# Optimization experiments

Hardware: AMD Instinct MI355X
Metric: run time of the kernel (lower is better)

Reference implementation:

```python
import jax, jax.numpy as jnp
import numpy as np
from jax import lax

CH = 256          # channels
FACTOR = 32       # EMA groups
CG = CH // FACTOR # channels per group = 8
B = 8             # number of point-cloud segments (batch)
NPTS = 32768      # points per segment (equal-length segments)
N = B * NPTS
EPS = 1e-5        # GroupNorm eps
FUSION_W = 0.1


def setup_inputs() -> dict:
    key = jax.random.key(0)
    ks = jax.random.split(key, 6)
    feat = jax.random.normal(ks[0], (N, CH), dtype=jnp.float32)
    # cumulative offsets of equal-length segments
    offset = ((jnp.arange(B, dtype=jnp.int32) + 1) * NPTS)
    s1 = 1.0 / np.sqrt(CG)      # torch Conv1d default init scale (fan_in=CG*k)
    s3 = 1.0 / np.sqrt(CG * 3)
    conv1_w = jax.random.uniform(ks[1], (CG, CG, 1), jnp.float32, -s1, s1)
    conv1_b = jax.random.uniform(ks[2], (CG,), jnp.float32, -s1, s1)
    conv3_w = jax.random.uniform(ks[3], (CG, CG, 3), jnp.float32, -s3, s3)
    conv3_b = jax.random.uniform(ks[4], (CG,), jnp.float32, -s3, s3)
    gn_w = jnp.ones((CG,), jnp.float32)
    gn_b = jnp.zeros((CG,), jnp.float32)
    fusion_weight = jnp.float32(FUSION_W)
    return {"feat": feat, "conv1_w": conv1_w, "conv1_b": conv1_b,
            "conv3_w": conv3_w, "conv3_b": conv3_b,
            "gn_w": gn_w, "gn_b": gn_b,
            "fusion_weight": fusion_weight, "offset": offset}


def _ema(x, conv1_w, conv1_b, conv3_w, conv3_b, gn_w, gn_b):
    # x: [BG, CG, n]  (BG = B * FACTOR)
    x_g = x.mean(-1, keepdims=True)                                   # agp -> [BG, CG, 1]
    x_g = jnp.einsum('oi,bis->bos', conv1_w[:, :, 0], x_g) + conv1_b[None, :, None]
    h = x * jax.nn.sigmoid(x_g)
    # GroupNorm(CG, CG): per-channel normalization over the point axis
    mu = h.mean(-1, keepdims=True)
    var = h.var(-1, keepdims=True)
    x1 = (h - mu) * lax.rsqrt(var + EPS) * gn_w[None, :, None] + gn_b[None, :, None]
    # conv3x3 along points, padding 1
    x2 = lax.conv_general_dilated(x, conv3_w, (1,), [(1, 1)],
                                  dimension_numbers=('NCH', 'OIH', 'NCH'))
    x2 = x2 + conv3_b[None, :, None]
    x11 = jax.nn.softmax(x1.mean(-1), axis=-1)                        # [BG, CG]
    x21 = jax.nn.softmax(x2.mean(-1), axis=-1)                        # [BG, CG]
    w = jnp.einsum('bc,bcn->bn', x11, x2) + jnp.einsum('bc,bcn->bn', x21, x1)
    return x * jax.nn.sigmoid(w)[:, None, :]


def reference(feat, conv1_w, conv1_b, conv3_w, conv3_b, gn_w, gn_b, fusion_weight, offset):
    # equal-length segments: [N, CH] -> [B, CH, NPTS]
    x = feat.reshape(B, NPTS, CH).transpose(0, 2, 1)
    gx = x.reshape(B * FACTOR, CG, NPTS)
    x_ema = _ema(gx, conv1_w, conv1_b, conv3_w, conv3_b, gn_w, gn_b).reshape(B, CH, NPTS)
    out = x + fusion_weight * (x_ema - x)      # residual fusion
    return out.transpose(0, 2, 1).reshape(N, CH)
```

## Files before the change

### kernel.cpp

```cpp
#include <hip/hip_runtime.h>
#include <math.h>

#define NSEG 8
#define NPTS 32768
#define CH   256
#define CG   8
#define EPS_GN 1e-5f


__global__ __launch_bounds__(256) void k_zero(float* __restrict__ acc) {
  acc[blockIdx.x * 256 + threadIdx.x] = 0.0f;
}

__global__ __launch_bounds__(256) void k_reduce(const float* __restrict__ feat,
                                                float* __restrict__ accS,
                                                float* __restrict__ accS2) {
  const int blk   = blockIdx.x;
  const int seg   = blk >> 7;
  const int chunk = blk & 127;
  const int q  = threadIdx.x & 63;
  const int dr = threadIdx.x >> 6;
  const float4* f4 = (const float4*)feat;
  const size_t rowbase = (size_t)seg * NPTS + (size_t)chunk * 256;
  float4 s  = make_float4(0.f, 0.f, 0.f, 0.f);
  float4 s2 = make_float4(0.f, 0.f, 0.f, 0.f);
  for (int r = dr; r < 256; r += 4) {
    float4 v = f4[(rowbase + r) * (CH / 4) + q];
    s.x += v.x;     s.y += v.y;     s.z += v.z;     s.w += v.w;
    s2.x += v.x*v.x; s2.y += v.y*v.y; s2.z += v.z*v.z; s2.w += v.w*v.w;
  }
  __shared__ float4 rs[256];
  __shared__ float4 rq[256];
  rs[threadIdx.x] = s;
  rq[threadIdx.x] = s2;
  __syncthreads();
  if (threadIdx.x < 64) {
    float4 a = rs[q], b = rs[64 + q], c = rs[128 + q], d = rs[192 + q];
    float4 e = rq[q], f = rq[64 + q], g = rq[128 + q], h = rq[192 + q];
    float sx = a.x + b.x + c.x + d.x;
    float sy = a.y + b.y + c.y + d.y;
    float sz = a.z + b.z + c.z + d.z;
    float sw = a.w + b.w + c.w + d.w;
    float tx = e.x + f.x + g.x + h.x;
    float ty = e.y + f.y + g.y + h.y;
    float tz = e.z + f.z + g.z + h.z;
    float tw = e.w + f.w + g.w + h.w;
    float* pS  = accS  + seg * CH + q * 4;
    float* pS2 = accS2 + seg * CH + q * 4;
    atomicAdd(pS + 0, sx);  atomicAdd(pS + 1, sy);
    atomicAdd(pS + 2, sz);  atomicAdd(pS + 3, sw);
    atomicAdd(pS2 + 0, tx); atomicAdd(pS2 + 1, ty);
    atomicAdd(pS2 + 2, tz); atomicAdd(pS2 + 3, tw);
  }
}

__global__ __launch_bounds__(256) void k_coef(const float* __restrict__ feat,
                                              const float* __restrict__ accS,
                                              const float* __restrict__ accS2,
                                              const float* __restrict__ c1w,
                                              const float* __restrict__ c1b,
                                              const float* __restrict__ c3w,
                                              const float* __restrict__ c3b,
                                              const float* __restrict__ gnw,
                                              const float* __restrict__ gnb,
                                              float* __restrict__ coeff) {
  const int gb  = threadIdx.x;
  const int seg = gb >> 5;
  const int g   = gb & 31;
  const float invn = 1.0f / (float)NPTS;

  float S[8], S2[8], mean[8], var[8];
#pragma unroll
  for (int i = 0; i < 8; ++i) {
    S[i]  = accS [seg * CH + g * 8 + i];
    S2[i] = accS2[seg * CH + g * 8 + i];
    mean[i] = S[i] * invn;
    var[i]  = fmaxf(S2[i] * invn - mean[i] * mean[i], 0.0f);
  }
  float xf[8], xl[8];
  const size_t rowf = ((size_t)seg * NPTS) * CH + g * 8;
  const size_t rowl = ((size_t)seg * NPTS + (NPTS - 1)) * CH + g * 8;
#pragma unroll
  for (int i = 0; i < 8; ++i) { xf[i] = feat[rowf + i]; xl[i] = feat[rowl + i]; }

  float a1[8];
#pragma unroll
  for (int o = 0; o < 8; ++o) {
    float xg = c1b[o];
#pragma unroll
    for (int i = 0; i < 8; ++i) xg += c1w[o * 8 + i] * mean[i];
    float gate = 1.0f / (1.0f + expf(-xg));
    float inv  = rsqrtf(gate * gate * var[o] + EPS_GN);
    a1[o] = gate * inv * gnw[o];
  }

  float x2m[8];
#pragma unroll
  for (int o = 0; o < 8; ++o) {
    float t = 0.0f;
#pragma unroll
    for (int i = 0; i < 8; ++i) {
      const float w0 = c3w[o * 24 + i * 3 + 0];
      const float w1 = c3w[o * 24 + i * 3 + 1];
      const float w2 = c3w[o * 24 + i * 3 + 2];
      t += w0 * (S[i] - xl[i]) + w1 * S[i] + w2 * (S[i] - xf[i]);
    }
    x2m[o] = c3b[o] + t * invn;
  }

  float x11[8], x21[8];
  {
    float m1 = gnb[0], m2 = x2m[0];
#pragma unroll
    for (int o = 1; o < 8; ++o) { m1 = fmaxf(m1, gnb[o]); m2 = fmaxf(m2, x2m[o]); }
    float d1 = 0.0f, d2 = 0.0f;
#pragma unroll
    for (int o = 0; o < 8; ++o) {
      x11[o] = expf(gnb[o] - m1); d1 += x11[o];
      x21[o] = expf(x2m[o] - m2); d2 += x21[o];
    }
    d1 = 1.0f / d1; d2 = 1.0f / d2;
#pragma unroll
    for (int o = 0; o < 8; ++o) { x11[o] *= d1; x21[o] *= d2; }
  }

  float P[8], Q[8], R[8];
#pragma unroll
  for (int i = 0; i < 8; ++i) {
    float p = 0.0f, qc = 0.0f, rr = 0.0f;
#pragma unroll
    for (int o = 0; o < 8; ++o) {
      const float s11 = x11[o];
      p  += s11 * c3w[o * 24 + i * 3 + 0];
      qc += s11 * c3w[o * 24 + i * 3 + 1];
      rr += s11 * c3w[o * 24 + i * 3 + 2];
    }
    P[i] = p; Q[i] = qc + x21[i] * a1[i]; R[i] = rr;
  }
  float K = 0.0f;
#pragma unroll
  for (int o = 0; o < 8; ++o)
    K += x11[o] * c3b[o] + x21[o] * (gnb[o] - a1[o] * mean[o]);

  float* cp = coeff + gb * 32;
  cp[0] = K;
#pragma unroll
  for (int i = 0; i < 8; ++i) { cp[4 + i] = P[i]; cp[12 + i] = Q[i]; cp[20 + i] = R[i]; }
}

__global__ __launch_bounds__(256) void k_main(const float* __restrict__ feat,
                                              const float* __restrict__ coeff,
                                              const float* __restrict__ fwp,
                                              float* __restrict__ out) {
  const int blk   = blockIdx.x;
  const int seg   = blk >> 8;
  const int chunk = blk & 255;
  const int g  = threadIdx.x & 31;
  const int dr = threadIdx.x >> 5;
  const int gb = seg * 32 + g;

  const float4* cp = (const float4*)(coeff + gb * 32);
  const float4 c0 = cp[0];
  const float4 P0 = cp[1], P1 = cp[2];
  const float4 Q0 = cp[3], Q1 = cp[4];
  const float4 R0 = cp[5], R1 = cp[6];
  const float K  = c0.x;
  const float fw = fwp[0];
  const float w1 = 1.0f - fw;

  const int r0 = chunk * 128;
  for (int r = r0 + dr; r < r0 + 128; r += 8) {
    const size_t row = (size_t)seg * NPTS + r;
    const float4* xp0 = (const float4*)(feat + row * CH + g * 8);
    const float4 a0 = xp0[0], a1 = xp0[1];
    float w = K
      + Q0.x * a0.x + Q0.y * a0.y + Q0.z * a0.z + Q0.w * a0.w
      + Q1.x * a1.x + Q1.y * a1.y + Q1.z * a1.z + Q1.w * a1.w;
    if (r > 0) {
      const float4* xm = xp0 - (CH / 4);
      const float4 m0 = xm[0], m1 = xm[1];
      w += P0.x * m0.x + P0.y * m0.y + P0.z * m0.z + P0.w * m0.w
         + P1.x * m1.x + P1.y * m1.y + P1.z * m1.z + P1.w * m1.w;
    }
    if (r < NPTS - 1) {
      const float4* xq = xp0 + (CH / 4);
      const float4 p0 = xq[0], p1 = xq[1];
      w += R0.x * p0.x + R0.y * p0.y + R0.z * p0.z + R0.w * p0.w
         + R1.x * p1.x + R1.y * p1.y + R1.z * p1.z + R1.w * p1.w;
    }
    const float sig   = 1.0f / (1.0f + __expf(-w));
    const float scale = w1 + fw * sig;
    float4 o0 = make_float4(a0.x * scale, a0.y * scale, a0.z * scale, a0.w * scale);
    float4 o1 = make_float4(a1.x * scale, a1.y * scale, a1.z * scale, a1.w * scale);
    float4* op = (float4*)(out + row * CH + g * 8);
    op[0] = o0; op[1] = o1;
  }
}

extern "C" void kernel_launch(void* const* d_in, const int* in_sizes, int n_in,
                              void* d_out, int out_size, void* d_ws, size_t ws_size,
                              hipStream_t stream) {
  const float* feat = (const float*)d_in[0];
  const float* c1w  = (const float*)d_in[1];
  const float* c1b  = (const float*)d_in[2];
  const float* c3w  = (const float*)d_in[3];
  const float* c3b  = (const float*)d_in[4];
  const float* gnw  = (const float*)d_in[5];
  const float* gnb  = (const float*)d_in[6];
  const float* fwp  = (const float*)d_in[7];
  float* out = (float*)d_out;
  float* ws  = (float*)d_ws;
  float* accS  = ws;
  float* accS2 = ws + NSEG * CH;
  float* coeff = ws + 2 * NSEG * CH;

  k_zero  <<<16,   256, 0, stream>>>(ws);
  k_reduce<<<1024, 256, 0, stream>>>(feat, accS, accS2);
  k_coef  <<<1,    256, 0, stream>>>(feat, accS, accS2, c1w, c1b, c3w, c3b, gnw, gnb, coeff);
  k_main  <<<2048, 256, 0, stream>>>(feat, coeff, fwp, out);
}
```

Before: 567.4 us.

## Replace atomic reduction with partial sums and stream rows with neighbor reuse

The reduction kernel now writes per-block partial sums to workspace instead of issuing atomics, which removes the zeroing kernel. A parallel coefficient kernel with one block per segment then sums those partials. The main kernel gives each thread a run of 16 consecutive rows and carries the previous and next row's dot products in registers, so each row is loaded about once rather than three times. The cost is a 4 MB partial buffer, a serial 256-step loop in the coefficient kernel, and access patterns where each warp touches different rows.

```diff
diff --git a/kernel.cpp b/kernel.cpp
--- a/kernel.cpp
+++ b/kernel.cpp
@@ -4,30 +4,27 @@
 #define NSEG 8
 #define NPTS 32768
 #define CH   256
-#define CG   8
 #define EPS_GN 1e-5f
 
 
-__global__ __launch_bounds__(256) void k_zero(float* __restrict__ acc) {
-  acc[blockIdx.x * 256 + threadIdx.x] = 0.0f;
+__device__ __forceinline__ float dot8(float4 a0, float4 a1, float4 b0, float4 b1) {
+  return a0.x * b0.x + a0.y * b0.y + a0.z * b0.z + a0.w * b0.w
+       + a1.x * b1.x + a1.y * b1.y + a1.z * b1.z + a1.w * b1.w;
 }
 
 __global__ __launch_bounds__(256) void k_reduce(const float* __restrict__ feat,
-                                                float* __restrict__ accS,
-                                                float* __restrict__ accS2) {
-  const int blk   = blockIdx.x;
-  const int seg   = blk >> 7;
-  const int chunk = blk & 127;
+                                                float* __restrict__ part) {
+  const int blk = blockIdx.x;
   const int q  = threadIdx.x & 63;
   const int dr = threadIdx.x >> 6;
   const float4* f4 = (const float4*)feat;
-  const size_t rowbase = (size_t)seg * NPTS + (size_t)chunk * 256;
+  const size_t rowbase = (size_t)blk * 128;
   float4 s  = make_float4(0.f, 0.f, 0.f, 0.f);
   float4 s2 = make_float4(0.f, 0.f, 0.f, 0.f);
-  for (int r = dr; r < 256; r += 4) {
+  for (int r = dr; r < 128; r += 4) {
     float4 v = f4[(rowbase + r) * (CH / 4) + q];
-    s.x += v.x;     s.y += v.y;     s.z += v.z;     s.w += v.w;
-    s2.x += v.x*v.x; s2.y += v.y*v.y; s2.z += v.z*v.z; s2.w += v.w*v.w;
+    s.x  += v.x;       s.y  += v.y;       s.z  += v.z;       s.w  += v.w;
+    s2.x += v.x * v.x; s2.y += v.y * v.y; s2.z += v.z * v.z; s2.w += v.w * v.w;
   }
   __shared__ float4 rs[256];
   __shared__ float4 rq[256];
@@ -37,26 +34,18 @@
   if (threadIdx.x < 64) {
     float4 a = rs[q], b = rs[64 + q], c = rs[128 + q], d = rs[192 + q];
     float4 e = rq[q], f = rq[64 + q], g = rq[128 + q], h = rq[192 + q];
-    float sx = a.x + b.x + c.x + d.x;
-    float sy = a.y + b.y + c.y + d.y;
-    float sz = a.z + b.z + c.z + d.z;
-    float sw = a.w + b.w + c.w + d.w;
-    float tx = e.x + f.x + g.x + h.x;
-    float ty = e.y + f.y + g.y + h.y;
-    float tz = e.z + f.z + g.z + h.z;
-    float tw = e.w + f.w + g.w + h.w;
-    float* pS  = accS  + seg * CH + q * 4;
-    float* pS2 = accS2 + seg * CH + q * 4;
-    atomicAdd(pS + 0, sx);  atomicAdd(pS + 1, sy);
-    atomicAdd(pS + 2, sz);  atomicAdd(pS + 3, sw);
-    atomicAdd(pS2 + 0, tx); atomicAdd(pS2 + 1, ty);
-    atomicAdd(pS2 + 2, tz); atomicAdd(pS2 + 3, tw);
+    float4 S  = make_float4(a.x + b.x + c.x + d.x, a.y + b.y + c.y + d.y,
+                            a.z + b.z + c.z + d.z, a.w + b.w + c.w + d.w);
+    float4 S2 = make_float4(e.x + f.x + g.x + h.x, e.y + f.y + g.y + h.y,
+                            e.z + f.z + g.z + h.z, e.w + f.w + g.w + h.w);
+    float4* pp = (float4*)(part + (size_t)blk * 512);
+    pp[q]      = S;
+    pp[64 + q] = S2;
   }
 }
 
 __global__ __launch_bounds__(256) void k_coef(const float* __restrict__ feat,
-                                              const float* __restrict__ accS,
-                                              const float* __restrict__ accS2,
+                                              const float* __restrict__ part,
                                               const float* __restrict__ c1w,
                                               const float* __restrict__ c1b,
                                               const float* __restrict__ c3w,
@@ -64,88 +53,94 @@
                                               const float* __restrict__ gnw,
                                               const float* __restrict__ gnb,
                                               float* __restrict__ coeff) {
-  const int gb  = threadIdx.x;
-  const int seg = gb >> 5;
-  const int g   = gb & 31;
-  const float invn = 1.0f / (float)NPTS;
-
-  float S[8], S2[8], mean[8], var[8];
-#pragma unroll
-  for (int i = 0; i < 8; ++i) {
-    S[i]  = accS [seg * CH + g * 8 + i];
-    S2[i] = accS2[seg * CH + g * 8 + i];
-    mean[i] = S[i] * invn;
-    var[i]  = fmaxf(S2[i] * invn - mean[i] * mean[i], 0.0f);
-  }
-  float xf[8], xl[8];
-  const size_t rowf = ((size_t)seg * NPTS) * CH + g * 8;
-  const size_t rowl = ((size_t)seg * NPTS + (NPTS - 1)) * CH + g * 8;
-#pragma unroll
-  for (int i = 0; i < 8; ++i) { xf[i] = feat[rowf + i]; xl[i] = feat[rowl + i]; }
-
-  float a1[8];
-#pragma unroll
-  for (int o = 0; o < 8; ++o) {
-    float xg = c1b[o];
-#pragma unroll
-    for (int i = 0; i < 8; ++i) xg += c1w[o * 8 + i] * mean[i];
-    float gate = 1.0f / (1.0f + expf(-xg));
-    float inv  = rsqrtf(gate * gate * var[o] + EPS_GN);
-    a1[o] = gate * inv * gnw[o];
-  }
-
-  float x2m[8];
-#pragma unroll
-  for (int o = 0; o < 8; ++o) {
-    float t = 0.0f;
+  const int seg = blockIdx.x;
+  const int c   = threadIdx.x;
+  const float* pb = part + (size_t)seg * 256 * 512;
+  float S = 0.0f, S2 = 0.0f;
+  for (int p = 0; p < 256; ++p) {
+    S  += pb[(size_t)p * 512 + c];
+    S2 += pb[(size_t)p * 512 + 256 + c];
+  }
+  __shared__ float sS[256], sS2[256], sxf[256], sxl[256];
+  sS[c]  = S;
+  sS2[c] = S2;
+  sxf[c] = feat[(size_t)seg * NPTS * CH + c];
+  sxl[c] = feat[((size_t)seg * NPTS + (NPTS - 1)) * CH + c];
+  __syncthreads();
+
+  if (c < 32) {
+    const int g = c;
+    const float invn = 1.0f / (float)NPTS;
+    float Ss[8], Q2[8], mean[8], var[8], xf[8], xl[8];
 #pragma unroll
     for (int i = 0; i < 8; ++i) {
-      const float w0 = c3w[o * 24 + i * 3 + 0];
-      const float w1 = c3w[o * 24 + i * 3 + 1];
-      const float w2 = c3w[o * 24 + i * 3 + 2];
-      t += w0 * (S[i] - xl[i]) + w1 * S[i] + w2 * (S[i] - xf[i]);
-    }
-    x2m[o] = c3b[o] + t * invn;
-  }
-
-  float x11[8], x21[8];
-  {
-    float m1 = gnb[0], m2 = x2m[0];
-#pragma unroll
-    for (int o = 1; o < 8; ++o) { m1 = fmaxf(m1, gnb[o]); m2 = fmaxf(m2, x2m[o]); }
-    float d1 = 0.0f, d2 = 0.0f;
+      Ss[i] = sS [g * 8 + i];
+      Q2[i] = sS2[g * 8 + i];
+      mean[i] = Ss[i] * invn;
+      var[i]  = fmaxf(Q2[i] * invn - mean[i] * mean[i], 0.0f);
+      xf[i] = sxf[g * 8 + i];
+      xl[i] = sxl[g * 8 + i];
+    }
+    float a1[8];
 #pragma unroll
     for (int o = 0; o < 8; ++o) {
-      x11[o] = expf(gnb[o] - m1); d1 += x11[o];
-      x21[o] = expf(x2m[o] - m2); d2 += x21[o];
-    }
-    d1 = 1.0f / d1; d2 = 1.0f / d2;
-#pragma unroll
-    for (int o = 0; o < 8; ++o) { x11[o] *= d1; x21[o] *= d2; }
-  }
-
-  float P[8], Q[8], R[8];
-#pragma unroll
-  for (int i = 0; i < 8; ++i) {
-    float p = 0.0f, qc = 0.0f, rr = 0.0f;
+      float xg = c1b[o];
+#pragma unroll
+      for (int i = 0; i < 8; ++i) xg += c1w[o * 8 + i] * mean[i];
+      float gate = 1.0f / (1.0f + expf(-xg));
+      a1[o] = gate * rsqrtf(gate * gate * var[o] + EPS_GN) * gnw[o];
+    }
+    float x2m[8];
 #pragma unroll
     for (int o = 0; o < 8; ++o) {
-      const float s11 = x11[o];
-      p  += s11 * c3w[o * 24 + i * 3 + 0];
-      qc += s11 * c3w[o * 24 + i * 3 + 1];
-      rr += s11 * c3w[o * 24 + i * 3 + 2];
-    }
-    P[i] = p; Q[i] = qc + x21[i] * a1[i]; R[i] = rr;
-  }
-  float K = 0.0f;
-#pragma unroll
-  for (int o = 0; o < 8; ++o)
-    K += x11[o] * c3b[o] + x21[o] * (gnb[o] - a1[o] * mean[o]);
-
-  float* cp = coeff + gb * 32;
-  cp[0] = K;
-#pragma unroll
-  for (int i = 0; i < 8; ++i) { cp[4 + i] = P[i]; cp[12 + i] = Q[i]; cp[20 + i] = R[i]; }
+      float t = 0.0f;
+#pragma unroll
+      for (int i = 0; i < 8; ++i) {
+        const float w0 = c3w[o * 24 + i * 3 + 0];
+        const float w1 = c3w[o * 24 + i * 3 + 1];
+        const float w2 = c3w[o * 24 + i * 3 + 2];
+        t += w0 * (Ss[i] - xl[i]) + w1 * Ss[i] + w2 * (Ss[i] - xf[i]);
+      }
+      x2m[o] = c3b[o] + t * invn;
+    }
+    float x11[8], x21[8];
+    {
+      float m1 = gnb[0], m2 = x2m[0];
+#pragma unroll
+      for (int o = 1; o < 8; ++o) { m1 = fmaxf(m1, gnb[o]); m2 = fmaxf(m2, x2m[o]); }
+      float d1 = 0.0f, d2 = 0.0f;
+#pragma unroll
+      for (int o = 0; o < 8; ++o) {
+        x11[o] = expf(gnb[o] - m1); d1 += x11[o];
+        x21[o] = expf(x2m[o] - m2); d2 += x21[o];
+      }
+      d1 = 1.0f / d1; d2 = 1.0f / d2;
+#pragma unroll
+      for (int o = 0; o < 8; ++o) { x11[o] *= d1; x21[o] *= d2; }
+    }
+    float P[8], Qc[8], R[8];
+#pragma unroll
+    for (int i = 0; i < 8; ++i) {
+      float p = 0.0f, qq = 0.0f, rr = 0.0f;
+#pragma unroll
+      for (int o = 0; o < 8; ++o) {
+        const float s11 = x11[o];
+        p  += s11 * c3w[o * 24 + i * 3 + 0];
+        qq += s11 * c3w[o * 24 + i * 3 + 1];
+        rr += s11 * c3w[o * 24 + i * 3 + 2];
+      }
+      P[i] = p; Qc[i] = qq + x21[i] * a1[i]; R[i] = rr;
+    }
+    float K = 0.0f;
+#pragma unroll
+    for (int o = 0; o < 8; ++o)
+      K += x11[o] * c3b[o] + x21[o] * (gnb[o] - a1[o] * mean[o]);
+
+    float* cpw = coeff + (seg * 32 + g) * 32;
+    cpw[0] = K;
+#pragma unroll
+    for (int i = 0; i < 8; ++i) { cpw[4 + i] = P[i]; cpw[12 + i] = Qc[i]; cpw[20 + i] = R[i]; }
+  }
 }
 
 __global__ __launch_bounds__(256) void k_main(const float* __restrict__ feat,
@@ -156,7 +151,7 @@
   const int seg   = blk >> 8;
   const int chunk = blk & 255;
   const int g  = threadIdx.x & 31;
-  const int dr = threadIdx.x >> 5;
+  const int tr = threadIdx.x >> 5;
   const int gb = seg * 32 + g;
 
   const float4* cp = (const float4*)(coeff + gb * 32);
@@ -168,32 +163,36 @@
   const float fw = fwp[0];
   const float w1 = 1.0f - fw;
 
-  const int r0 = chunk * 128;
-  for (int r = r0 + dr; r < r0 + 128; r += 8) {
-    const size_t row = (size_t)seg * NPTS + r;
-    const float4* xp0 = (const float4*)(feat + row * CH + g * 8);
-    const float4 a0 = xp0[0], a1 = xp0[1];
-    float w = K
-      + Q0.x * a0.x + Q0.y * a0.y + Q0.z * a0.z + Q0.w * a0.w
-      + Q1.x * a1.x + Q1.y * a1.y + Q1.z * a1.z + Q1.w * a1.w;
-    if (r > 0) {
-      const float4* xm = xp0 - (CH / 4);
-      const float4 m0 = xm[0], m1 = xm[1];
-      w += P0.x * m0.x + P0.y * m0.y + P0.z * m0.z + P0.w * m0.w
-         + P1.x * m1.x + P1.y * m1.y + P1.z * m1.z + P1.w * m1.w;
-    }
-    if (r < NPTS - 1) {
-      const float4* xq = xp0 + (CH / 4);
-      const float4 p0 = xq[0], p1 = xq[1];
-      w += R0.x * p0.x + R0.y * p0.y + R0.z * p0.z + R0.w * p0.w
-         + R1.x * p1.x + R1.y * p1.y + R1.z * p1.z + R1.w * p1.w;
-    }
-    const float sig   = 1.0f / (1.0f + __expf(-w));
-    const float scale = w1 + fw * sig;
-    float4 o0 = make_float4(a0.x * scale, a0.y * scale, a0.z * scale, a0.w * scale);
-    float4 o1 = make_float4(a1.x * scale, a1.y * scale, a1.z * scale, a1.w * scale);
-    float4* op = (float4*)(out + row * CH + g * 8);
-    op[0] = o0; op[1] = o1;
+  const int base = chunk * 128 + tr * 16;
+  const float4* f4 = (const float4*)feat;
+  float4* o4 = (float4*)out;
+  const size_t idx0 = ((size_t)seg * NPTS + base) * (CH / 4) + g * 2;
+
+  float dPprev = 0.0f;
+  if (base > 0) {
+    float4 m0 = f4[idx0 - 64], m1 = f4[idx0 - 63];
+    dPprev = dot8(P0, P1, m0, m1);
+  }
+  float4 xc0 = f4[idx0], xc1 = f4[idx0 + 1];
+  float dQc = dot8(Q0, Q1, xc0, xc1);
+
+#pragma unroll 4
+  for (int s = 0; s < 16; ++s) {
+    const size_t idx = idx0 + (size_t)s * 64;
+    float4 xn0 = xc0, xn1 = xc1;
+    float dRn = 0.0f;
+    if (base + s + 1 < NPTS) {
+      xn0 = f4[idx + 64];
+      xn1 = f4[idx + 65];
+      dRn = dot8(R0, R1, xn0, xn1);
+    }
+    const float w = K + dPprev + dQc + dRn;
+    const float scale = w1 + fw / (1.0f + __expf(-w));
+    o4[idx]     = make_float4(xc0.x * scale, xc0.y * scale, xc0.z * scale, xc0.w * scale);
+    o4[idx + 1] = make_float4(xc1.x * scale, xc1.y * scale, xc1.z * scale, xc1.w * scale);
+    dPprev = dot8(P0, P1, xc0, xc1);
+    dQc    = dot8(Q0, Q1, xn0, xn1);
+    xc0 = xn0; xc1 = xn1;
   }
 }
 
@@ -210,12 +209,10 @@
   const float* fwp  = (const float*)d_in[7];
   float* out = (float*)d_out;
   float* ws  = (float*)d_ws;
-  float* accS  = ws;
-  float* accS2 = ws + NSEG * CH;
-  float* coeff = ws + 2 * NSEG * CH;
-
-  k_zero  <<<16,   256, 0, stream>>>(ws);
-  k_reduce<<<1024, 256, 0, stream>>>(feat, accS, accS2);
-  k_coef  <<<1,    256, 0, stream>>>(feat, accS, accS2, c1w, c1b, c3w, c3b, gnw, gnb, coeff);
+  float* part  = ws;
+  float* coeff = ws + 2048 * 512;
+
+  k_reduce<<<2048, 256, 0, stream>>>(feat, part);
+  k_coef  <<<8,    256, 0, stream>>>(feat, part, c1w, c1b, c3w, c3b, gnw, gnb, coeff);
   k_main  <<<2048, 256, 0, stream>>>(feat, coeff, fwp, out);
 }
```

New measurement: 541.7 us. -4.5%, faster.
